# Performance work log

Hardware: AMD Instinct MI355X
Metric: run time of the kernel (lower is better)

Reference implementation:

```python
import jax, jax.numpy as jnp
import numpy as np

N_NODES = 100000
N_EDGES = 3200000
IN_CH, HID, OUT_CH = 256, 64, 64


def setup_inputs() -> dict:
    key = jax.random.key(0)
    k1, k2, k3, k4 = jax.random.split(key, 4)
    x = jax.random.normal(k1, (N_NODES, IN_CH), dtype=jnp.float32)
    edge_index = jax.random.randint(k2, (2, N_EDGES), 0, N_NODES, dtype=jnp.int64)
    W1 = jax.random.normal(k3, (IN_CH, HID), dtype=jnp.float32) * (1.0 / np.sqrt(IN_CH))
    b1 = jnp.zeros((HID,), dtype=jnp.float32)
    W2 = jax.random.normal(k4, (HID, OUT_CH), dtype=jnp.float32) * (1.0 / np.sqrt(HID))
    b2 = jnp.zeros((OUT_CH,), dtype=jnp.float32)
    return {"x": x, "edge_index": edge_index, "W1": W1, "b1": b1, "W2": W2, "b2": b2}


def reference(x, edge_index, W1, b1, W2, b2):
    N = x.shape[0]
    # GCN normalization: add self-loops, deg^{-1/2} on both endpoints
    loops = jnp.arange(N, dtype=edge_index.dtype)
    src = jnp.concatenate([edge_index[0], loops])
    dst = jnp.concatenate([edge_index[1], loops])
    deg = jax.ops.segment_sum(jnp.ones(src.shape, x.dtype), dst, num_segments=N)
    dinv = jnp.where(deg > 0, jax.lax.rsqrt(deg), 0.0)
    norm = dinv[src] * dinv[dst]  # [E+N]

    def gcn(h, W, b):
        h = h @ W  # dense linear transform
        # gather-scale-scatter aggregation over edges
        agg = jax.ops.segment_sum(h[src] * norm[:, None], dst, num_segments=N)
        return agg + b

    h = jax.nn.relu(gcn(x, W1, b1))
    return gcn(h, W2, b2)
```

## Files before the change

kernel.cpp:

```cpp
#include <hip/hip_runtime.h>

typedef unsigned short u16;
typedef unsigned int u32;
typedef __bf16 bf16x8 __attribute__((ext_vector_type(8)));
typedef float f32x4 __attribute__((ext_vector_type(4)));
typedef u16 u16x8 __attribute__((ext_vector_type(8)));

#define IN_CH 256
#define HID 64
#define BSHIFT 8
#define BNODES 256
#define NBUK 391
#define BCAP 10240
#define TILE 8192

__device__ __forceinline__ u16 f2bf(float f) {
  union { float f; unsigned u; } v; v.f = f;
  unsigned r = v.u + 0x7FFFu + ((v.u >> 16) & 1u);
  return (u16)(r >> 16);
}
__device__ __forceinline__ float bf2f(u16 h) {
  union { unsigned u; float f; } v; v.u = ((unsigned)h) << 16;
  return v.f;
}

__global__ void k_wprep(const float* __restrict__ W1, const float* __restrict__ W2,
                        u16* __restrict__ w1t, u16* __restrict__ w2t) {
  int t = blockIdx.x * blockDim.x + threadIdx.x;
  if (t < 64 * 256) {
    int n = t >> 8, k = t & 255;
    w1t[t] = f2bf(W1[k * 64 + n]);
  }
  int t2 = t - 64 * 256;
  if (t2 >= 0 && t2 < 64 * 64) {
    int n = t2 >> 6, k = t2 & 63;
    w2t[t2] = f2bf(W2[k * 64 + n]);
  }
}


__global__ __launch_bounds__(1024) void k_part(const int* __restrict__ e_src,
                                               const int* __restrict__ e_dst,
                                               int* __restrict__ bcnt,
                                               u32* __restrict__ bedge, int E) {
  __shared__ int lcnt[512];
  __shared__ int lscan[512];
  __shared__ int gbase[512];
  __shared__ int wsum[8];
  __shared__ u32 stag[TILE];
  __shared__ int dest[TILE];
  int t = threadIdx.x;
  int base = blockIdx.x * TILE;
  int here = E - base; if (here > TILE) here = TILE;

  if (t < 512) lcnt[t] = 0;
  __syncthreads();

  u32 m[8]; int bk[8]; int rk[8];
#pragma unroll
  for (int k = 0; k < 8; ++k) {
    int e = base + t + k * 1024;
    if (e < E) {
      int s = e_src[e], d = e_dst[e];
      bk[k] = d >> BSHIFT;
      m[k] = (u32)s | ((u32)(d & (BNODES - 1)) << 20);
      rk[k] = atomicAdd(&lcnt[bk[k]], 1);
    } else bk[k] = -1;
  }
  __syncthreads();

  int lane = t & 63, w = t >> 6;
  int v = 0, x = 0;
  if (t < 512) { v = lcnt[t]; x = v; }
#pragma unroll
  for (int off = 1; off < 64; off <<= 1) {
    int y = __shfl_up(x, off);
    if (lane >= off) x += y;
  }
  if (t < 512 && lane == 63) wsum[w] = x;
  __syncthreads();
  if (t < 512) {
    int wo = 0;
    for (int i = 0; i < w; ++i) wo += wsum[i];
    lscan[t] = x - v + wo;
  }
  __syncthreads();

  if (t < NBUK) gbase[t] = t * BCAP + atomicAdd(&bcnt[t], lcnt[t]);
  __syncthreads();

#pragma unroll
  for (int k = 0; k < 8; ++k) {
    if (bk[k] >= 0) {
      int p = lscan[bk[k]] + rk[k];
      stag[p] = m[k];
      dest[p] = gbase[bk[k]] + rk[k];
    }
  }
  __syncthreads();

#pragma unroll
  for (int k = 0; k < 8; ++k) {
    int p = t + k * 1024;
    if (p < here) bedge[dest[p]] = stag[p];
  }
}


__global__ __launch_bounds__(1024) void k_sort(const int* __restrict__ bcnt,
                                               u32* __restrict__ bedge,
                                               int* __restrict__ rptr,
                                               int* __restrict__ rcnt,
                                               float* __restrict__ dinv, int N) {
  __shared__ u32 stag[BCAP];
  __shared__ int hist[BNODES];
  __shared__ int cur[BNODES];
  __shared__ int wsum4[4];
  int b = blockIdx.x, t = threadIdx.x;
  if (t < BNODES) hist[t] = 0;
  __syncthreads();
  int n = bcnt[b]; if (n > BCAP) n = BCAP;
  u32* be = bedge + (size_t)b * BCAP;

  for (int i = t; i < n; i += 1024) atomicAdd(&hist[be[i] >> 20], 1);
  __syncthreads();

  int lane = t & 63, w = t >> 6;
  int v = 0, x = 0;
  if (t < BNODES) { v = hist[t]; x = v; }
#pragma unroll
  for (int off = 1; off < 64; off <<= 1) {
    int y = __shfl_up(x, off);
    if (lane >= off) x += y;
  }
  if (t < BNODES && lane == 63) wsum4[w] = x;
  __syncthreads();
  if (t < BNODES) {
    int wo = 0;
    for (int i = 0; i < w; ++i) wo += wsum4[i];
    int ex = x - v + wo;
    cur[t] = ex;
    int node = (b << BSHIFT) + t;
    if (node < N) {
      rptr[node] = b * BCAP + ex;
      rcnt[node] = v;
      dinv[node] = rsqrtf((float)(v + 1));
    }
  }
  __syncthreads();

  for (int i = t; i < n; i += 1024) {
    u32 m = be[i];
    int p = atomicAdd(&cur[m >> 20], 1);
    stag[p] = m;
  }
  __syncthreads();

  for (int i = t; i < n; i += 1024) be[i] = stag[i];
}


__global__ __launch_bounds__(256, 1) void k_gemm1(const float* __restrict__ x,
                                                  const u16* __restrict__ w1t,
                                                  const float* __restrict__ dinv,
                                                  u16* __restrict__ h1, int N) {
  int lane = threadIdx.x & 63;
  int wave = threadIdx.x >> 6;
  int rowbase = (blockIdx.x * 4 + wave) * 16;
  if (rowbase >= N) return;
  int mn = lane & 15, quad = lane >> 4;
  const float* arow = x + (size_t)(rowbase + mn) * IN_CH + quad * 8;

  float4 a[16];
#pragma unroll
  for (int kc = 0; kc < 8; ++kc) {
    a[2 * kc] = *(const float4*)(arow + kc * 32);
    a[2 * kc + 1] = *(const float4*)(arow + kc * 32 + 4);
  }
  u16x8 au[8];
#pragma unroll
  for (int kc = 0; kc < 8; ++kc) {
    float4 a0 = a[2 * kc], a1 = a[2 * kc + 1];
    au[kc][0] = f2bf(a0.x); au[kc][1] = f2bf(a0.y);
    au[kc][2] = f2bf(a0.z); au[kc][3] = f2bf(a0.w);
    au[kc][4] = f2bf(a1.x); au[kc][5] = f2bf(a1.y);
    au[kc][6] = f2bf(a1.z); au[kc][7] = f2bf(a1.w);
  }

  f32x4 acc[4] = {{0.f, 0.f, 0.f, 0.f}, {0.f, 0.f, 0.f, 0.f},
                  {0.f, 0.f, 0.f, 0.f}, {0.f, 0.f, 0.f, 0.f}};
#pragma unroll
  for (int c = 0; c < 4; ++c) {
    const u16* brow = w1t + (c * 16 + mn) * IN_CH + quad * 8;
    u16x8 bu[8];
#pragma unroll
    for (int kc = 0; kc < 8; ++kc) bu[kc] = *(const u16x8*)(brow + kc * 32);
#pragma unroll
    for (int kc = 0; kc < 8; ++kc)
      acc[c] = __builtin_amdgcn_mfma_f32_16x16x32_bf16(
          __builtin_bit_cast(bf16x8, au[kc]), __builtin_bit_cast(bf16x8, bu[kc]),
          acc[c], 0, 0, 0);
  }
#pragma unroll
  for (int r = 0; r < 4; ++r) {
    int row = rowbase + quad * 4 + r;
    float dv = dinv[row];
#pragma unroll
    for (int c = 0; c < 4; ++c)
      h1[(size_t)row * HID + c * 16 + mn] = f2bf(dv * acc[c][r]);
  }
}

__global__ __launch_bounds__(256) void k_gemm2(const u16* __restrict__ g1,
                                               const u16* __restrict__ w2t,
                                               const float* __restrict__ dinv,
                                               u16* __restrict__ h2) {
  int lane = threadIdx.x & 63;
  int wave = threadIdx.x >> 6;
  int rowbase = blockIdx.x * 16;
  int colbase = wave * 16;
  int mn = lane & 15, quad = lane >> 4;
  const u16* arow = g1 + (size_t)(rowbase + mn) * HID + quad * 8;
  const u16* brow = w2t + (colbase + mn) * HID + quad * 8;
  u16x8 au0 = *(const u16x8*)(arow);
  u16x8 au1 = *(const u16x8*)(arow + 32);
  u16x8 bu0 = *(const u16x8*)(brow);
  u16x8 bu1 = *(const u16x8*)(brow + 32);
  f32x4 acc = {0.f, 0.f, 0.f, 0.f};
  acc = __builtin_amdgcn_mfma_f32_16x16x32_bf16(
      __builtin_bit_cast(bf16x8, au0), __builtin_bit_cast(bf16x8, bu0), acc, 0, 0, 0);
  acc = __builtin_amdgcn_mfma_f32_16x16x32_bf16(
      __builtin_bit_cast(bf16x8, au1), __builtin_bit_cast(bf16x8, bu1), acc, 0, 0, 0);
#pragma unroll
  for (int r = 0; r < 4; ++r) {
    int row = rowbase + quad * 4 + r;
    h2[(size_t)row * HID + colbase + mn] = f2bf(dinv[row] * acc[r]);
  }
}


template <bool RELU, bool BF16OUT>
__global__ __launch_bounds__(256, 4) void k_agg(const u16* __restrict__ hin,
                                                const int* __restrict__ rptr,
                                                const int* __restrict__ rcnt,
                                                const u32* __restrict__ sedge,
                                                const float* __restrict__ bias,
                                                void* __restrict__ outv, int N) {
  int wid = blockIdx.x * 4 + (threadIdx.x >> 6);
  int lane = threadIdx.x & 63;
  if (wid >= N) return;
  int start = __builtin_amdgcn_readfirstlane(rptr[wid]);
  int len = __builtin_amdgcn_readfirstlane(rcnt[wid]);
  float di = rsqrtf((float)(len + 1));
  float a0 = bf2f(hin[(size_t)wid * HID + lane]);
  float a1 = 0.f, a2 = 0.f, a3 = 0.f;
  const u32* se = sedge + start;
  int j = 0;
  for (; j + 16 <= len; j += 16) {
    u16 v[16];
#pragma unroll
    for (int k = 0; k < 16; ++k) {
      int e = (int)(se[j + k] & 0xFFFFF);
      v[k] = hin[(size_t)e * HID + lane];
    }
#pragma unroll
    for (int k = 0; k < 16; ++k) {
      float f = bf2f(v[k]);
      if ((k & 3) == 0) a0 += f;
      else if ((k & 3) == 1) a1 += f;
      else if ((k & 3) == 2) a2 += f;
      else a3 += f;
    }
  }
  if (j + 8 <= len) {
    u16 v[8];
#pragma unroll
    for (int k = 0; k < 8; ++k) {
      int e = (int)(se[j + k] & 0xFFFFF);
      v[k] = hin[(size_t)e * HID + lane];
    }
#pragma unroll
    for (int k = 0; k < 8; ++k) {
      float f = bf2f(v[k]);
      if ((k & 3) == 0) a0 += f;
      else if ((k & 3) == 1) a1 += f;
      else if ((k & 3) == 2) a2 += f;
      else a3 += f;
    }
    j += 8;
  }
  if (j + 4 <= len) {
    u16 v[4];
#pragma unroll
    for (int k = 0; k < 4; ++k) {
      int e = (int)(se[j + k] & 0xFFFFF);
      v[k] = hin[(size_t)e * HID + lane];
    }
    a0 += bf2f(v[0]); a1 += bf2f(v[1]); a2 += bf2f(v[2]); a3 += bf2f(v[3]);
    j += 4;
  }
  for (; j < len; ++j) {
    int e = (int)(se[j] & 0xFFFFF);
    a0 += bf2f(hin[(size_t)e * HID + lane]);
  }
  float acc = (a0 + a1) + (a2 + a3);
  acc = di * acc + bias[lane];
  if (RELU) acc = fmaxf(acc, 0.f);
  if (BF16OUT) ((u16*)outv)[(size_t)wid * HID + lane] = f2bf(acc);
  else ((float*)outv)[(size_t)wid * HID + lane] = acc;
}


extern "C" void kernel_launch(void* const* d_in, const int* in_sizes, int n_in,
                              void* d_out, int out_size, void* d_ws, size_t ws_size,
                              hipStream_t stream) {
  const float* x = (const float*)d_in[0];
  const int* ei = (const int*)d_in[1];
  const float* W1 = (const float*)d_in[2];
  const float* b1 = (const float*)d_in[3];
  const float* W2 = (const float*)d_in[4];
  const float* b2 = (const float*)d_in[5];
  float* out = (float*)d_out;

  const int N = in_sizes[0] / IN_CH;
  const int E = in_sizes[1] / 2;
  const int* e_src = ei;
  const int* e_dst = ei + E;

  size_t off = 0;
  auto carve = [&](size_t bytes) -> char* {
    char* p = (char*)d_ws + off;
    off += (bytes + 255) & ~(size_t)255;
    return p;
  };
  int* bcnt = (int*)carve((size_t)NBUK * 4);
  u32* bedge = (u32*)carve((size_t)NBUK * BCAP * 4);
  int* rptr = (int*)carve((size_t)N * 4);
  int* rcnt = (int*)carve((size_t)N * 4);
  float* dinv = (float*)carve((size_t)N * 4);
  u16* w1t = (u16*)carve(64 * 256 * 2);
  u16* w2t = (u16*)carve(64 * 64 * 2);
  u16* h1 = (u16*)carve((size_t)N * HID * 2);
  u16* g1 = (u16*)carve((size_t)N * HID * 2);

  const int n_tiles = (E + TILE - 1) / TILE;
  const int nb_g1 = (N + 63) / 64;

  hipMemsetAsync(bcnt, 0, (size_t)NBUK * 4, stream);
  k_wprep<<<(64 * 256 + 64 * 64 + 255) / 256, 256, 0, stream>>>(W1, W2, w1t, w2t);
  k_part<<<n_tiles, 1024, 0, stream>>>(e_src, e_dst, bcnt, bedge, E);
  k_sort<<<NBUK, 1024, 0, stream>>>(bcnt, bedge, rptr, rcnt, dinv, N);
  k_gemm1<<<nb_g1, 256, 0, stream>>>(x, w1t, dinv, h1, N);
  k_agg<true, true><<<(N + 3) / 4, 256, 0, stream>>>(h1, rptr, rcnt, bedge, b1, g1, N);
  k_gemm2<<<N / 16, 256, 0, stream>>>(g1, w2t, dinv, h1);
  k_agg<false, false><<<(N + 3) / 4, 256, 0, stream>>>(h1, rptr, rcnt, bedge, b2, out, N);
}
```

Before: 346.8 us.

## Split aggregation wave into four edge groups with 8-byte vector row loads

The aggregation kernel now has each wavefront process four edges at once. Each 16-lane group loads a full 64-channel bf16 row in 8-byte chunks, instead of all 64 lanes reading 2-byte elements of one edge at a time. Partial sums are combined with cross-lane shuffles, and one group applies the self term, bias, relu and a vectorized store. This cuts the number of load instructions and keeps more independent row fetches in flight per wave. The cost is shuffle reductions and masked tail handling for edge counts that are not a multiple of four.

```diff
diff --git a/kernel.cpp b/kernel.cpp
--- a/kernel.cpp
+++ b/kernel.cpp
@@ -5,6 +5,7 @@
 typedef __bf16 bf16x8 __attribute__((ext_vector_type(8)));
 typedef float f32x4 __attribute__((ext_vector_type(4)));
 typedef u16 u16x8 __attribute__((ext_vector_type(8)));
+typedef u16 u16x4 __attribute__((ext_vector_type(4)));
 
 #define IN_CH 256
 #define HID 64
@@ -249,65 +250,72 @@
   int wid = blockIdx.x * 4 + (threadIdx.x >> 6);
   int lane = threadIdx.x & 63;
   if (wid >= N) return;
+  int grp = lane >> 4;
+  int cb = lane & 15;
   int start = __builtin_amdgcn_readfirstlane(rptr[wid]);
   int len = __builtin_amdgcn_readfirstlane(rcnt[wid]);
   float di = rsqrtf((float)(len + 1));
-  float a0 = bf2f(hin[(size_t)wid * HID + lane]);
-  float a1 = 0.f, a2 = 0.f, a3 = 0.f;
+  u16x4 sv = *(const u16x4*)(hin + (size_t)wid * HID + (cb << 2));
+  float acc0 = 0.f, acc1 = 0.f, acc2 = 0.f, acc3 = 0.f;
   const u32* se = sedge + start;
   int j = 0;
-  for (; j + 16 <= len; j += 16) {
-    u16 v[16];
-#pragma unroll
-    for (int k = 0; k < 16; ++k) {
-      int e = (int)(se[j + k] & 0xFFFFF);
-      v[k] = hin[(size_t)e * HID + lane];
-    }
-#pragma unroll
-    for (int k = 0; k < 16; ++k) {
-      float f = bf2f(v[k]);
-      if ((k & 3) == 0) a0 += f;
-      else if ((k & 3) == 1) a1 += f;
-      else if ((k & 3) == 2) a2 += f;
-      else a3 += f;
-    }
-  }
-  if (j + 8 <= len) {
-    u16 v[8];
-#pragma unroll
-    for (int k = 0; k < 8; ++k) {
-      int e = (int)(se[j + k] & 0xFFFFF);
-      v[k] = hin[(size_t)e * HID + lane];
-    }
-#pragma unroll
-    for (int k = 0; k < 8; ++k) {
-      float f = bf2f(v[k]);
-      if ((k & 3) == 0) a0 += f;
-      else if ((k & 3) == 1) a1 += f;
-      else if ((k & 3) == 2) a2 += f;
-      else a3 += f;
-    }
-    j += 8;
-  }
-  if (j + 4 <= len) {
-    u16 v[4];
-#pragma unroll
-    for (int k = 0; k < 4; ++k) {
-      int e = (int)(se[j + k] & 0xFFFFF);
-      v[k] = hin[(size_t)e * HID + lane];
-    }
-    a0 += bf2f(v[0]); a1 += bf2f(v[1]); a2 += bf2f(v[2]); a3 += bf2f(v[3]);
-    j += 4;
-  }
-  for (; j < len; ++j) {
-    int e = (int)(se[j] & 0xFFFFF);
-    a0 += bf2f(hin[(size_t)e * HID + lane]);
-  }
-  float acc = (a0 + a1) + (a2 + a3);
-  acc = di * acc + bias[lane];
-  if (RELU) acc = fmaxf(acc, 0.f);
-  if (BF16OUT) ((u16*)outv)[(size_t)wid * HID + lane] = f2bf(acc);
-  else ((float*)outv)[(size_t)wid * HID + lane] = acc;
+  for (; j + 32 <= len; j += 32) {
+    u16x4 v[8];
+#pragma unroll
+    for (int p = 0; p < 8; ++p) {
+      u32 w = se[j + p * 4 + grp];
+      v[p] = *(const u16x4*)(hin + (size_t)(w & 0xFFFFF) * HID + (cb << 2));
+    }
+#pragma unroll
+    for (int p = 0; p < 8; ++p) {
+      acc0 += bf2f(v[p][0]); acc1 += bf2f(v[p][1]);
+      acc2 += bf2f(v[p][2]); acc3 += bf2f(v[p][3]);
+    }
+  }
+  if (j + 16 <= len) {
+    u16x4 v[4];
+#pragma unroll
+    for (int p = 0; p < 4; ++p) {
+      u32 w = se[j + p * 4 + grp];
+      v[p] = *(const u16x4*)(hin + (size_t)(w & 0xFFFFF) * HID + (cb << 2));
+    }
+#pragma unroll
+    for (int p = 0; p < 4; ++p) {
+      acc0 += bf2f(v[p][0]); acc1 += bf2f(v[p][1]);
+      acc2 += bf2f(v[p][2]); acc3 += bf2f(v[p][3]);
+    }
+    j += 16;
+  }
+  for (; j < len; j += 4) {
+    int idx = j + grp;
+    u32 w = se[idx < len ? idx : len - 1];
+    u16x4 v = *(const u16x4*)(hin + (size_t)(w & 0xFFFFF) * HID + (cb << 2));
+    float m = idx < len ? 1.f : 0.f;
+    acc0 = fmaf(m, bf2f(v[0]), acc0); acc1 = fmaf(m, bf2f(v[1]), acc1);
+    acc2 = fmaf(m, bf2f(v[2]), acc2); acc3 = fmaf(m, bf2f(v[3]), acc3);
+  }
+  acc0 += __shfl_xor(acc0, 16); acc0 += __shfl_xor(acc0, 32);
+  acc1 += __shfl_xor(acc1, 16); acc1 += __shfl_xor(acc1, 32);
+  acc2 += __shfl_xor(acc2, 16); acc2 += __shfl_xor(acc2, 32);
+  acc3 += __shfl_xor(acc3, 16); acc3 += __shfl_xor(acc3, 32);
+  if (grp == 0) {
+    acc0 += bf2f(sv[0]); acc1 += bf2f(sv[1]);
+    acc2 += bf2f(sv[2]); acc3 += bf2f(sv[3]);
+    float4 bv = *(const float4*)(bias + (cb << 2));
+    acc0 = di * acc0 + bv.x; acc1 = di * acc1 + bv.y;
+    acc2 = di * acc2 + bv.z; acc3 = di * acc3 + bv.w;
+    if (RELU) {
+      acc0 = fmaxf(acc0, 0.f); acc1 = fmaxf(acc1, 0.f);
+      acc2 = fmaxf(acc2, 0.f); acc3 = fmaxf(acc3, 0.f);
+    }
+    if (BF16OUT) {
+      u16x4 o = {f2bf(acc0), f2bf(acc1), f2bf(acc2), f2bf(acc3)};
+      *(u16x4*)((u16*)outv + (size_t)wid * HID + (cb << 2)) = o;
+    } else {
+      float4 o = {acc0, acc1, acc2, acc3};
+      *((float4*)outv + (size_t)wid * (HID / 4) + cb) = o;
+    }
+  }
 }
 
 
```

Result: slower. 362.5 us (+4.6%).

## Reorder layer-2 aggregation before W2 transform and fuse GEMM2 into aggregation

Applied to the files above, without the earlier changes.

Because aggregation is linear, layer 2 now aggregates the 64-wide dinv-scaled hidden features first and applies W2 afterwards. The W2 matmul is done in the aggregation kernel through a shared-memory row buffer, and the bias is added at the end. This removes the separate gemm2 kernel, one launch, and one full write and read of the N×64 intermediate. In exchange each 1024-thread block converts W2 to bf16 into LDS, and the per-row matmul runs as scalar FMAs with LDS reads rather than MFMA.

```diff
diff --git a/kernel.cpp b/kernel.cpp
--- a/kernel.cpp
+++ b/kernel.cpp
@@ -24,17 +24,11 @@
   return v.f;
 }
 
-__global__ void k_wprep(const float* __restrict__ W1, const float* __restrict__ W2,
-                        u16* __restrict__ w1t, u16* __restrict__ w2t) {
+__global__ void k_wprep(const float* __restrict__ W1, u16* __restrict__ w1t) {
   int t = blockIdx.x * blockDim.x + threadIdx.x;
   if (t < 64 * 256) {
     int n = t >> 8, k = t & 255;
     w1t[t] = f2bf(W1[k * 64 + n]);
-  }
-  int t2 = t - 64 * 256;
-  if (t2 >= 0 && t2 < 64 * 64) {
-    int n = t2 >> 6, k = t2 & 63;
-    w2t[t2] = f2bf(W2[k * 64 + n]);
   }
 }
 
@@ -211,41 +205,13 @@
   }
 }
 
-__global__ __launch_bounds__(256) void k_gemm2(const u16* __restrict__ g1,
-                                               const u16* __restrict__ w2t,
-                                               const float* __restrict__ dinv,
-                                               u16* __restrict__ h2) {
-  int lane = threadIdx.x & 63;
-  int wave = threadIdx.x >> 6;
-  int rowbase = blockIdx.x * 16;
-  int colbase = wave * 16;
-  int mn = lane & 15, quad = lane >> 4;
-  const u16* arow = g1 + (size_t)(rowbase + mn) * HID + quad * 8;
-  const u16* brow = w2t + (colbase + mn) * HID + quad * 8;
-  u16x8 au0 = *(const u16x8*)(arow);
-  u16x8 au1 = *(const u16x8*)(arow + 32);
-  u16x8 bu0 = *(const u16x8*)(brow);
-  u16x8 bu1 = *(const u16x8*)(brow + 32);
-  f32x4 acc = {0.f, 0.f, 0.f, 0.f};
-  acc = __builtin_amdgcn_mfma_f32_16x16x32_bf16(
-      __builtin_bit_cast(bf16x8, au0), __builtin_bit_cast(bf16x8, bu0), acc, 0, 0, 0);
-  acc = __builtin_amdgcn_mfma_f32_16x16x32_bf16(
-      __builtin_bit_cast(bf16x8, au1), __builtin_bit_cast(bf16x8, bu1), acc, 0, 0, 0);
-#pragma unroll
-  for (int r = 0; r < 4; ++r) {
-    int row = rowbase + quad * 4 + r;
-    h2[(size_t)row * HID + colbase + mn] = f2bf(dinv[row] * acc[r]);
-  }
-}
-
-
-template <bool RELU, bool BF16OUT>
-__global__ __launch_bounds__(256, 4) void k_agg(const u16* __restrict__ hin,
-                                                const int* __restrict__ rptr,
-                                                const int* __restrict__ rcnt,
-                                                const u32* __restrict__ sedge,
-                                                const float* __restrict__ bias,
-                                                void* __restrict__ outv, int N) {
+
+__global__ __launch_bounds__(256, 4) void k_agg1(const u16* __restrict__ hin,
+                                                 const int* __restrict__ rptr,
+                                                 const int* __restrict__ rcnt,
+                                                 const u32* __restrict__ sedge,
+                                                 const float* __restrict__ bias,
+                                                 u16* __restrict__ outu, int N) {
   int wid = blockIdx.x * 4 + (threadIdx.x >> 6);
   int lane = threadIdx.x & 63;
   if (wid >= N) return;
@@ -305,9 +271,88 @@
   }
   float acc = (a0 + a1) + (a2 + a3);
   acc = di * acc + bias[lane];
-  if (RELU) acc = fmaxf(acc, 0.f);
-  if (BF16OUT) ((u16*)outv)[(size_t)wid * HID + lane] = f2bf(acc);
-  else ((float*)outv)[(size_t)wid * HID + lane] = acc;
+  acc = fmaxf(acc, 0.f);
+  outu[(size_t)wid * HID + lane] = f2bf(di * acc);
+}
+
+
+__global__ __launch_bounds__(1024, 4) void k_agg2(const u16* __restrict__ u1,
+                                                  const int* __restrict__ rptr,
+                                                  const int* __restrict__ rcnt,
+                                                  const u32* __restrict__ sedge,
+                                                  const float* __restrict__ W2,
+                                                  const float* __restrict__ b2,
+                                                  float* __restrict__ out, int N) {
+  __shared__ u16 w2s[HID * HID];
+  __shared__ float rowbuf[16][HID];
+  int t = threadIdx.x;
+  for (int i = t; i < HID * HID; i += 1024) w2s[i] = f2bf(W2[i]);
+  __syncthreads();
+  int wave = t >> 6, lane = t & 63;
+  int wid = blockIdx.x * 16 + wave;
+  if (wid >= N) return;
+  int start = __builtin_amdgcn_readfirstlane(rptr[wid]);
+  int len = __builtin_amdgcn_readfirstlane(rcnt[wid]);
+  float di = rsqrtf((float)(len + 1));
+  float a0 = bf2f(u1[(size_t)wid * HID + lane]);
+  float a1 = 0.f, a2 = 0.f, a3 = 0.f;
+  const u32* se = sedge + start;
+  int j = 0;
+  for (; j + 16 <= len; j += 16) {
+    u16 v[16];
+#pragma unroll
+    for (int k = 0; k < 16; ++k) {
+      int e = (int)(se[j + k] & 0xFFFFF);
+      v[k] = u1[(size_t)e * HID + lane];
+    }
+#pragma unroll
+    for (int k = 0; k < 16; ++k) {
+      float f = bf2f(v[k]);
+      if ((k & 3) == 0) a0 += f;
+      else if ((k & 3) == 1) a1 += f;
+      else if ((k & 3) == 2) a2 += f;
+      else a3 += f;
+    }
+  }
+  if (j + 8 <= len) {
+    u16 v[8];
+#pragma unroll
+    for (int k = 0; k < 8; ++k) {
+      int e = (int)(se[j + k] & 0xFFFFF);
+      v[k] = u1[(size_t)e * HID + lane];
+    }
+#pragma unroll
+    for (int k = 0; k < 8; ++k) {
+      float f = bf2f(v[k]);
+      if ((k & 3) == 0) a0 += f;
+      else if ((k & 3) == 1) a1 += f;
+      else if ((k & 3) == 2) a2 += f;
+      else a3 += f;
+    }
+    j += 8;
+  }
+  if (j + 4 <= len) {
+    u16 v[4];
+#pragma unroll
+    for (int k = 0; k < 4; ++k) {
+      int e = (int)(se[j + k] & 0xFFFFF);
+      v[k] = u1[(size_t)e * HID + lane];
+    }
+    a0 += bf2f(v[0]); a1 += bf2f(v[1]); a2 += bf2f(v[2]); a3 += bf2f(v[3]);
+    j += 4;
+  }
+  for (; j < len; ++j) {
+    int e = (int)(se[j] & 0xFFFFF);
+    a0 += bf2f(u1[(size_t)e * HID + lane]);
+  }
+  float acc = (a0 + a1) + (a2 + a3);
+
+  rowbuf[wave][lane] = acc;
+  float o = 0.f;
+#pragma unroll 8
+  for (int k = 0; k < HID; ++k)
+    o += rowbuf[wave][k] * bf2f(w2s[k * HID + lane]);
+  out[(size_t)wid * HID + lane] = di * o + b2[lane];
 }
 
 
@@ -339,19 +384,17 @@
   int* rcnt = (int*)carve((size_t)N * 4);
   float* dinv = (float*)carve((size_t)N * 4);
   u16* w1t = (u16*)carve(64 * 256 * 2);
-  u16* w2t = (u16*)carve(64 * 64 * 2);
   u16* h1 = (u16*)carve((size_t)N * HID * 2);
-  u16* g1 = (u16*)carve((size_t)N * HID * 2);
+  u16* u1 = (u16*)carve((size_t)N * HID * 2);
 
   const int n_tiles = (E + TILE - 1) / TILE;
   const int nb_g1 = (N + 63) / 64;
 
   hipMemsetAsync(bcnt, 0, (size_t)NBUK * 4, stream);
-  k_wprep<<<(64 * 256 + 64 * 64 + 255) / 256, 256, 0, stream>>>(W1, W2, w1t, w2t);
+  k_wprep<<<(64 * 256 + 255) / 256, 256, 0, stream>>>(W1, w1t);
   k_part<<<n_tiles, 1024, 0, stream>>>(e_src, e_dst, bcnt, bedge, E);
   k_sort<<<NBUK, 1024, 0, stream>>>(bcnt, bedge, rptr, rcnt, dinv, N);
   k_gemm1<<<nb_g1, 256, 0, stream>>>(x, w1t, dinv, h1, N);
-  k_agg<true, true><<<(N + 3) / 4, 256, 0, stream>>>(h1, rptr, rcnt, bedge, b1, g1, N);
-  k_gemm2<<<N / 16, 256, 0, stream>>>(g1, w2t, dinv, h1);
-  k_agg<false, false><<<(N + 3) / 4, 256, 0, stream>>>(h1, rptr, rcnt, bedge, b2, out, N);
-}
+  k_agg1<<<(N + 3) / 4, 256, 0, stream>>>(h1, rptr, rcnt, bedge, b1, u1, N);
+  k_agg2<<<(N + 15) / 16, 1024, 0, stream>>>(u1, rptr, rcnt, bedge, W2, b2, out, N);
+}
```

Measured after the change: 359.5 us. 1.04x slower.

## Replace bucketed partition+sort CSR build with global histogram and atomic scatter

Applied to the files above, without the earlier changes.

Replaces the two-pass bucket partition and in-bucket counting sort with three simple kernels: a global-atomic degree histogram, a per-bucket scan that writes row pointers, and an atomic-cursor scatter of source indices into per-node slots. The aggregation kernel now takes the row length from the final cursor value and uses the raw source index without masking. This removes the shared-memory staging and the extra read/write pass over the edge buffer. In exchange it relies on heavy global atomics with scattered 4-byte writes, and edge order within each row becomes nondeterministic.

```diff
diff --git a/kernel.cpp b/kernel.cpp
--- a/kernel.cpp
+++ b/kernel.cpp
@@ -12,7 +12,6 @@
 #define BNODES 256
 #define NBUK 391
 #define BCAP 10240
-#define TILE 8192
 
 __device__ __forceinline__ u16 f2bf(float f) {
   union { float f; unsigned u; } v; v.f = f;
@@ -39,124 +38,63 @@
 }
 
 
-__global__ __launch_bounds__(1024) void k_part(const int* __restrict__ e_src,
-                                               const int* __restrict__ e_dst,
-                                               int* __restrict__ bcnt,
-                                               u32* __restrict__ bedge, int E) {
-  __shared__ int lcnt[512];
-  __shared__ int lscan[512];
-  __shared__ int gbase[512];
-  __shared__ int wsum[8];
-  __shared__ u32 stag[TILE];
-  __shared__ int dest[TILE];
-  int t = threadIdx.x;
-  int base = blockIdx.x * TILE;
-  int here = E - base; if (here > TILE) here = TILE;
-
-  if (t < 512) lcnt[t] = 0;
-  __syncthreads();
-
-  u32 m[8]; int bk[8]; int rk[8];
-#pragma unroll
-  for (int k = 0; k < 8; ++k) {
-    int e = base + t + k * 1024;
-    if (e < E) {
-      int s = e_src[e], d = e_dst[e];
-      bk[k] = d >> BSHIFT;
-      m[k] = (u32)s | ((u32)(d & (BNODES - 1)) << 20);
-      rk[k] = atomicAdd(&lcnt[bk[k]], 1);
-    } else bk[k] = -1;
-  }
-  __syncthreads();
-
+__global__ __launch_bounds__(256) void k_hist(const int* __restrict__ e_dst,
+                                              int* __restrict__ hist, int E4) {
+  int t = blockIdx.x * blockDim.x + threadIdx.x;
+  if (t < E4) {
+    int4 d = ((const int4*)e_dst)[t];
+    atomicAdd(&hist[d.x], 1);
+    atomicAdd(&hist[d.y], 1);
+    atomicAdd(&hist[d.z], 1);
+    atomicAdd(&hist[d.w], 1);
+  }
+}
+
+__global__ __launch_bounds__(256) void k_rptr(const int* __restrict__ hist,
+                                              int* __restrict__ rptr,
+                                              int* __restrict__ cur,
+                                              float* __restrict__ dinv, int N) {
+  __shared__ int wsum[4];
+  int b = blockIdx.x, t = threadIdx.x;
+  int node = (b << BSHIFT) + t;
+  int v = (node < N) ? hist[node] : 0;
   int lane = t & 63, w = t >> 6;
-  int v = 0, x = 0;
-  if (t < 512) { v = lcnt[t]; x = v; }
+  int x = v;
 #pragma unroll
   for (int off = 1; off < 64; off <<= 1) {
     int y = __shfl_up(x, off);
     if (lane >= off) x += y;
   }
-  if (t < 512 && lane == 63) wsum[w] = x;
+  if (lane == 63) wsum[w] = x;
   __syncthreads();
-  if (t < 512) {
-    int wo = 0;
-    for (int i = 0; i < w; ++i) wo += wsum[i];
-    lscan[t] = x - v + wo;
-  }
-  __syncthreads();
-
-  if (t < NBUK) gbase[t] = t * BCAP + atomicAdd(&bcnt[t], lcnt[t]);
-  __syncthreads();
-
-#pragma unroll
-  for (int k = 0; k < 8; ++k) {
-    if (bk[k] >= 0) {
-      int p = lscan[bk[k]] + rk[k];
-      stag[p] = m[k];
-      dest[p] = gbase[bk[k]] + rk[k];
-    }
-  }
-  __syncthreads();
-
-#pragma unroll
-  for (int k = 0; k < 8; ++k) {
-    int p = t + k * 1024;
-    if (p < here) bedge[dest[p]] = stag[p];
-  }
-}
-
-
-__global__ __launch_bounds__(1024) void k_sort(const int* __restrict__ bcnt,
-                                               u32* __restrict__ bedge,
-                                               int* __restrict__ rptr,
-                                               int* __restrict__ rcnt,
-                                               float* __restrict__ dinv, int N) {
-  __shared__ u32 stag[BCAP];
-  __shared__ int hist[BNODES];
-  __shared__ int cur[BNODES];
-  __shared__ int wsum4[4];
-  int b = blockIdx.x, t = threadIdx.x;
-  if (t < BNODES) hist[t] = 0;
-  __syncthreads();
-  int n = bcnt[b]; if (n > BCAP) n = BCAP;
-  u32* be = bedge + (size_t)b * BCAP;
-
-  for (int i = t; i < n; i += 1024) atomicAdd(&hist[be[i] >> 20], 1);
-  __syncthreads();
-
-  int lane = t & 63, w = t >> 6;
-  int v = 0, x = 0;
-  if (t < BNODES) { v = hist[t]; x = v; }
-#pragma unroll
-  for (int off = 1; off < 64; off <<= 1) {
-    int y = __shfl_up(x, off);
-    if (lane >= off) x += y;
-  }
-  if (t < BNODES && lane == 63) wsum4[w] = x;
-  __syncthreads();
-  if (t < BNODES) {
-    int wo = 0;
-    for (int i = 0; i < w; ++i) wo += wsum4[i];
-    int ex = x - v + wo;
-    cur[t] = ex;
-    int node = (b << BSHIFT) + t;
-    if (node < N) {
-      rptr[node] = b * BCAP + ex;
-      rcnt[node] = v;
-      dinv[node] = rsqrtf((float)(v + 1));
-    }
-  }
-  __syncthreads();
-
-  for (int i = t; i < n; i += 1024) {
-    u32 m = be[i];
-    int p = atomicAdd(&cur[m >> 20], 1);
-    stag[p] = m;
-  }
-  __syncthreads();
-
-  for (int i = t; i < n; i += 1024) be[i] = stag[i];
+  int wo = 0;
+  for (int i = 0; i < w; ++i) wo += wsum[i];
+  int ex = x - v + wo;
+  if (node < N) {
+    int p = b * BCAP + ex;
+    rptr[node] = p;
+    cur[node] = p;
+    dinv[node] = rsqrtf((float)(v + 1));
+  }
+}
+
+__global__ __launch_bounds__(256) void k_scatter(const int* __restrict__ e_src,
+                                                 const int* __restrict__ e_dst,
+                                                 int* __restrict__ cur,
+                                                 u32* __restrict__ sedge, int E4) {
+  int t = blockIdx.x * blockDim.x + threadIdx.x;
+  if (t < E4) {
+    int4 d = ((const int4*)e_dst)[t];
+    int4 s = ((const int4*)e_src)[t];
+    int p0 = atomicAdd(&cur[d.x], 1);
+    int p1 = atomicAdd(&cur[d.y], 1);
+    int p2 = atomicAdd(&cur[d.z], 1);
+    int p3 = atomicAdd(&cur[d.w], 1);
+    sedge[p0] = (u32)s.x;
+    sedge[p1] = (u32)s.y;
+    sedge[p2] = (u32)s.z;
+    sedge[p3] = (u32)s.w;
+  }
 }
 
 
@@ -242,7 +180,7 @@
 template <bool RELU, bool BF16OUT>
 __global__ __launch_bounds__(256, 4) void k_agg(const u16* __restrict__ hin,
                                                 const int* __restrict__ rptr,
-                                                const int* __restrict__ rcnt,
+                                                const int* __restrict__ cur,
                                                 const u32* __restrict__ sedge,
                                                 const float* __restrict__ bias,
                                                 void* __restrict__ outv, int N) {
@@ -250,7 +188,7 @@
   int lane = threadIdx.x & 63;
   if (wid >= N) return;
   int start = __builtin_amdgcn_readfirstlane(rptr[wid]);
-  int len = __builtin_amdgcn_readfirstlane(rcnt[wid]);
+  int len = __builtin_amdgcn_readfirstlane(cur[wid]) - start;
   float di = rsqrtf((float)(len + 1));
   float a0 = bf2f(hin[(size_t)wid * HID + lane]);
   float a1 = 0.f, a2 = 0.f, a3 = 0.f;
@@ -260,7 +198,7 @@
     u16 v[16];
 #pragma unroll
     for (int k = 0; k < 16; ++k) {
-      int e = (int)(se[j + k] & 0xFFFFF);
+      int e = (int)se[j + k];
       v[k] = hin[(size_t)e * HID + lane];
     }
 #pragma unroll
@@ -276,7 +214,7 @@
     u16 v[8];
 #pragma unroll
     for (int k = 0; k < 8; ++k) {
-      int e = (int)(se[j + k] & 0xFFFFF);
+      int e = (int)se[j + k];
       v[k] = hin[(size_t)e * HID + lane];
     }
 #pragma unroll
@@ -293,14 +231,14 @@
     u16 v[4];
 #pragma unroll
     for (int k = 0; k < 4; ++k) {
-      int e = (int)(se[j + k] & 0xFFFFF);
+      int e = (int)se[j + k];
       v[k] = hin[(size_t)e * HID + lane];
     }
     a0 += bf2f(v[0]); a1 += bf2f(v[1]); a2 += bf2f(v[2]); a3 += bf2f(v[3]);
     j += 4;
   }
   for (; j < len; ++j) {
-    int e = (int)(se[j] & 0xFFFFF);
+    int e = (int)se[j];
     a0 += bf2f(hin[(size_t)e * HID + lane]);
   }
   float acc = (a0 + a1) + (a2 + a3);
@@ -333,25 +271,27 @@
     off += (bytes + 255) & ~(size_t)255;
     return p;
   };
-  int* bcnt = (int*)carve((size_t)NBUK * 4);
-  u32* bedge = (u32*)carve((size_t)NBUK * BCAP * 4);
+  int* hist = (int*)carve((size_t)N * 4);
   int* rptr = (int*)carve((size_t)N * 4);
-  int* rcnt = (int*)carve((size_t)N * 4);
+  int* cur = (int*)carve((size_t)N * 4);
   float* dinv = (float*)carve((size_t)N * 4);
+  u32* sedge = (u32*)carve((size_t)NBUK * BCAP * 4);
   u16* w1t = (u16*)carve(64 * 256 * 2);
   u16* w2t = (u16*)carve(64 * 64 * 2);
   u16* h1 = (u16*)carve((size_t)N * HID * 2);
   u16* g1 = (u16*)carve((size_t)N * HID * 2);
 
-  const int n_tiles = (E + TILE - 1) / TILE;
+  const int E4 = E / 4;
+  const int nb_e4 = (E4 + 255) / 256;
   const int nb_g1 = (N + 63) / 64;
 
-  hipMemsetAsync(bcnt, 0, (size_t)NBUK * 4, stream);
+  (void)hipMemsetAsync(hist, 0, (size_t)N * 4, stream);
   k_wprep<<<(64 * 256 + 64 * 64 + 255) / 256, 256, 0, stream>>>(W1, W2, w1t, w2t);
-  k_part<<<n_tiles, 1024, 0, stream>>>(e_src, e_dst, bcnt, bedge, E);
-  k_sort<<<NBUK, 1024, 0, stream>>>(bcnt, bedge, rptr, rcnt, dinv, N);
+  k_hist<<<nb_e4, 256, 0, stream>>>(e_dst, hist, E4);
+  k_rptr<<<NBUK, 256, 0, stream>>>(hist, rptr, cur, dinv, N);
+  k_scatter<<<nb_e4, 256, 0, stream>>>(e_src, e_dst, cur, sedge, E4);
   k_gemm1<<<nb_g1, 256, 0, stream>>>(x, w1t, dinv, h1, N);
-  k_agg<true, true><<<(N + 3) / 4, 256, 0, stream>>>(h1, rptr, rcnt, bedge, b1, g1, N);
+  k_agg<true, true><<<(N + 3) / 4, 256, 0, stream>>>(h1, rptr, cur, sedge, b1, g1, N);
   k_gemm2<<<N / 16, 256, 0, stream>>>(g1, w2t, dinv, h1);
-  k_agg<false, false><<<(N + 3) / 4, 256, 0, stream>>>(h1, rptr, rcnt, bedge, b2, out, N);
-}
+  k_agg<false, false><<<(N + 3) / 4, 256, 0, stream>>>(h1, rptr, cur, sedge, b2, out, N);
+}
```

After: 722.0 us. +108.2%, slower.
